# Optimization experiments

Measured on AMD Instinct MI355X. Metric: run time of the kernel, lower is better.

The kernel has to match this reference:

```python
import jax, jax.numpy as jnp
import numpy as np

N, IN_C, HID, OUT_C = 100000, 512, 256, 32
E = 1_600_000
K, LAM1, LAM2 = 5, 3.0, 3.0  # elastic prop hyperparams


def setup_inputs() -> dict:
    key = jax.random.key(0)
    ks = jax.random.split(key, 6)
    x = jax.random.normal(ks[0], (N, IN_C), dtype=jnp.float32)
    edge_index = jax.random.randint(ks[1], (2, E), 0, N, dtype=jnp.int64)
    s1 = 1.0 / np.sqrt(IN_C)
    s2 = 1.0 / np.sqrt(HID)
    W1 = jax.random.uniform(ks[2], (IN_C, HID), jnp.float32, -s1, s1)
    b1 = jax.random.uniform(ks[3], (HID,), jnp.float32, -s1, s1)
    W2 = jax.random.uniform(ks[4], (HID, OUT_C), jnp.float32, -s2, s2)
    b2 = jax.random.uniform(ks[5], (OUT_C,), jnp.float32, -s2, s2)
    return dict(x=x, edge_index=edge_index, W1=W1, b1=b1, W2=W2, b2=b2)


def _emp(h, row, col):
    """Elastic Message Passing (ElasticGNN): proximal-gradient iterations over
    the degree-normalized incidence operator with L1 dual projection."""
    n = h.shape[0]
    deg = jnp.zeros((n,), h.dtype).at[row].add(1.0).at[col].add(1.0)
    dis = jax.lax.rsqrt(jnp.maximum(deg, 1.0))  # 1/sqrt(deg)
    dr = dis[row][:, None]  # [E,1]
    dc = dis[col][:, None]
    gamma = 1.0 / (1.0 + LAM2)
    beta = 1.0 / (2.0 * gamma)

    def step(carry, _):
        z, y = carry
        # dual ascent on edge variables: z += beta * (Delta y), then project
        # onto the L-inf ball of radius lambda1 (prox of L1 penalty's dual)
        z = jnp.clip(z + beta * (y[row] * dr - y[col] * dc), -LAM1, LAM1)
        # primal: y = gamma * h - gamma * Delta^T z  (scatter back to nodes)
        atz = jnp.zeros_like(y).at[row].add(z * dr).at[col].add(-(z * dc))
        y = gamma * h - gamma * atz
        return (z, y), None

    z0 = jnp.zeros((row.shape[0], h.shape[1]), h.dtype)
    (z, y), _ = jax.lax.scan(step, (z0, gamma * h), None, length=K)
    return y


def reference(x, edge_index, W1, b1, W2, b2):
    # eval mode: dropout is identity
    h = jax.nn.relu(x @ W1 + b1)
    h = h @ W2 + b2                       # [N, OUT_C]
    row, col = edge_index[0], edge_index[1]
    y = _emp(h, row, col)                 # sparse elastic propagation
    return jax.nn.log_softmax(y, axis=1)
```

## Files before the change

### kernel.cpp

```cpp
#include <hip/hip_runtime.h>
#include <math.h>

#define IN_C  512
#define HID   256
#define OUT_C 32
#define GAMMA 0.25f
#define BETA  2.0f
#define LAM1  3.0f
#define ZS    10922.0f
#define ZSI   (1.0f / 10922.0f)

#define BM 128
#define BN 128
#define BK 16

__global__ __launch_bounds__(256) void gemm1_relu_kernel(
    const float* __restrict__ A, const float* __restrict__ B,
    const float* __restrict__ bias, float* __restrict__ C, int M)
{
    __shared__ float As[BK][BM + 4];
    __shared__ float Bs[BK][BN + 4];
    const int tid = threadIdx.x;
    const int bm = blockIdx.x * BM;
    const int bn = blockIdx.y * BN;
    const int tx = tid & 15;
    const int ty = tid >> 4;

    float acc[8][8];
#pragma unroll
    for (int i = 0; i < 8; ++i)
#pragma unroll
        for (int j = 0; j < 8; ++j) acc[i][j] = 0.f;

    const int a_row = tid >> 2;
    const int a_col = (tid & 3) << 2;
    const int b_row = tid >> 5;
    const int b_col = (tid & 31) << 2;

    for (int k0 = 0; k0 < IN_C; k0 += BK) {
#pragma unroll
        for (int r = 0; r < 2; ++r) {
            const int m = a_row + r * 64;
            const int gm = bm + m;
            float4 v = make_float4(0.f, 0.f, 0.f, 0.f);
            if (gm < M) v = *(const float4*)&A[(size_t)gm * IN_C + k0 + a_col];
            As[a_col + 0][m] = v.x;
            As[a_col + 1][m] = v.y;
            As[a_col + 2][m] = v.z;
            As[a_col + 3][m] = v.w;
        }
#pragma unroll
        for (int r = 0; r < 2; ++r) {
            const int kk = b_row + r * 8;
            *(float4*)&Bs[kk][b_col] =
                *(const float4*)&B[(size_t)(k0 + kk) * HID + bn + b_col];
        }
        __syncthreads();
#pragma unroll
        for (int kk = 0; kk < BK; ++kk) {
            float a[8], b[8];
            *(float4*)&a[0] = *(float4*)&As[kk][ty * 8];
            *(float4*)&a[4] = *(float4*)&As[kk][ty * 8 + 4];
            *(float4*)&b[0] = *(float4*)&Bs[kk][tx * 4];
            *(float4*)&b[4] = *(float4*)&Bs[kk][64 + tx * 4];
#pragma unroll
            for (int i = 0; i < 8; ++i)
#pragma unroll
                for (int j = 0; j < 8; ++j)
                    acc[i][j] = fmaf(a[i], b[j], acc[i][j]);
        }
        __syncthreads();
    }

#pragma unroll
    for (int i = 0; i < 8; ++i) {
        const int gm = bm + ty * 8 + i;
        if (gm >= M) continue;
#pragma unroll
        for (int g = 0; g < 2; ++g) {
            const int gn = bn + g * 64 + tx * 4;
            float4 v;
            v.x = fmaxf(acc[i][g * 4 + 0] + bias[gn + 0], 0.f);
            v.y = fmaxf(acc[i][g * 4 + 1] + bias[gn + 1], 0.f);
            v.z = fmaxf(acc[i][g * 4 + 2] + bias[gn + 2], 0.f);
            v.w = fmaxf(acc[i][g * 4 + 3] + bias[gn + 3], 0.f);
            *(float4*)&C[(size_t)gm * HID + gn] = v;
        }
    }
}

#define G2_ROWS 128
#define G2_KT   64

__global__ __launch_bounds__(256) void gemm2_kernel(
    const float* __restrict__ H1, const float* __restrict__ W2,
    const float* __restrict__ b2, float* __restrict__ H,
    float* __restrict__ Y, int M)
{
    __shared__ float W2s[HID * OUT_C];
    __shared__ float rows_s[G2_ROWS][G2_KT + 4];
    const int tid = threadIdx.x;
    const int brow = blockIdx.x * G2_ROWS;
    const int cg = tid & 7;
    const int rg = tid >> 3;

#pragma unroll
    for (int r = 0; r < 8; ++r)
        ((float4*)W2s)[tid + r * 256] = ((const float4*)W2)[tid + r * 256];

    float acc[4][4];
#pragma unroll
    for (int r = 0; r < 4; ++r)
#pragma unroll
        for (int c = 0; c < 4; ++c) acc[r][c] = 0.f;

    for (int k0 = 0; k0 < HID; k0 += G2_KT) {
        __syncthreads();
#pragma unroll
        for (int i = 0; i < 8; ++i) {
            const int idx = tid + i * 256;
            const int rl = idx >> 4;
            const int c4 = idx & 15;
            const int gr = brow + rl;
            float4 v = make_float4(0.f, 0.f, 0.f, 0.f);
            if (gr < M) v = *(const float4*)&H1[(size_t)gr * HID + k0 + c4 * 4];
            *(float4*)&rows_s[rl][c4 * 4] = v;
        }
        __syncthreads();
#pragma unroll
        for (int kq = 0; kq < G2_KT / 4; ++kq) {
            float4 w[4];
#pragma unroll
            for (int j = 0; j < 4; ++j)
                w[j] = ((const float4*)W2s)[(k0 + kq * 4 + j) * 8 + cg];
#pragma unroll
            for (int r = 0; r < 4; ++r) {
                const float4 rh = *(const float4*)&rows_s[rg * 4 + r][kq * 4];
                acc[r][0] = fmaf(rh.x, w[0].x, acc[r][0]);
                acc[r][1] = fmaf(rh.x, w[0].y, acc[r][1]);
                acc[r][2] = fmaf(rh.x, w[0].z, acc[r][2]);
                acc[r][3] = fmaf(rh.x, w[0].w, acc[r][3]);
                acc[r][0] = fmaf(rh.y, w[1].x, acc[r][0]);
                acc[r][1] = fmaf(rh.y, w[1].y, acc[r][1]);
                acc[r][2] = fmaf(rh.y, w[1].z, acc[r][2]);
                acc[r][3] = fmaf(rh.y, w[1].w, acc[r][3]);
                acc[r][0] = fmaf(rh.z, w[2].x, acc[r][0]);
                acc[r][1] = fmaf(rh.z, w[2].y, acc[r][1]);
                acc[r][2] = fmaf(rh.z, w[2].z, acc[r][2]);
                acc[r][3] = fmaf(rh.z, w[2].w, acc[r][3]);
                acc[r][0] = fmaf(rh.w, w[3].x, acc[r][0]);
                acc[r][1] = fmaf(rh.w, w[3].y, acc[r][1]);
                acc[r][2] = fmaf(rh.w, w[3].z, acc[r][2]);
                acc[r][3] = fmaf(rh.w, w[3].w, acc[r][3]);
            }
        }
    }

    const float4 bias = *(const float4*)&b2[cg * 4];
#pragma unroll
    for (int r = 0; r < 4; ++r) {
        const int grow = brow + rg * 4 + r;
        if (grow >= M) continue;
        float4 s;
        s.x = acc[r][0] + bias.x;
        s.y = acc[r][1] + bias.y;
        s.z = acc[r][2] + bias.z;
        s.w = acc[r][3] + bias.w;
        *(float4*)&H[(size_t)grow * OUT_C + cg * 4] = s;
        float4 y0;
        y0.x = GAMMA * s.x; y0.y = GAMMA * s.y;
        y0.z = GAMMA * s.z; y0.w = GAMMA * s.w;
        *(float4*)&Y[(size_t)grow * OUT_C + cg * 4] = y0;
    }
}

__global__ void hist2_kernel(const int* __restrict__ row, const int* __restrict__ col,
                             int* __restrict__ cnt_r, int* __restrict__ cnt_c, int E)
{
    const int t = blockIdx.x * blockDim.x + threadIdx.x;
    if (t >= E) return;
    atomicAdd(&cnt_r[row[t]], 1);
    atomicAdd(&cnt_c[col[t]], 1);
}

__global__ void dis_kernel(const int* __restrict__ cnt_r, const int* __restrict__ cnt_c,
                           float* __restrict__ dis, int N)
{
    const int t = blockIdx.x * blockDim.x + threadIdx.x;
    if (t < N) dis[t] = 1.f / sqrtf(fmaxf((float)(cnt_r[t] + cnt_c[t]), 1.f));
}

#define SCAN_CHUNK 1024

__global__ __launch_bounds__(256) void scan1_kernel(
    const int* __restrict__ counts, int* __restrict__ bsum, int N)
{
    __shared__ int sm[256];
    const int tid = threadIdx.x;
    const int base = blockIdx.x * SCAN_CHUNK + tid * 4;
    int s = 0;
#pragma unroll
    for (int i = 0; i < 4; ++i)
        if (base + i < N) s += counts[base + i];
    sm[tid] = s;
    __syncthreads();
    for (int off = 128; off; off >>= 1) {
        if (tid < off) sm[tid] += sm[tid + off];
        __syncthreads();
    }
    if (tid == 0) bsum[blockIdx.x] = sm[0];
}

__global__ void scan2_kernel(int* __restrict__ bsum, int* __restrict__ boff, int nb)
{
    if (threadIdx.x == 0 && blockIdx.x == 0) {
        int acc = 0;
        for (int i = 0; i < nb; ++i) { boff[i] = acc; acc += bsum[i]; }
    }
}

__global__ __launch_bounds__(256) void scan3_kernel(
    const int* __restrict__ counts, const int* __restrict__ boff,
    int* __restrict__ ptr, int* __restrict__ cursor, int N)
{
    __shared__ int sm[256];
    const int tid = threadIdx.x;
    const int base = blockIdx.x * SCAN_CHUNK + tid * 4;
    int c[4];
#pragma unroll
    for (int i = 0; i < 4; ++i)
        c[i] = (base + i < N) ? counts[base + i] : 0;
    const int tsum = c[0] + c[1] + c[2] + c[3];
    sm[tid] = tsum;
    __syncthreads();
    for (int off = 1; off < 256; off <<= 1) {
        int v = (tid >= off) ? sm[tid - off] : 0;
        __syncthreads();
        sm[tid] += v;
        __syncthreads();
    }
    int run = boff[blockIdx.x] + sm[tid] - tsum;
#pragma unroll
    for (int i = 0; i < 4; ++i) {
        if (base + i < N) {
            ptr[base + i] = run;
            cursor[base + i] = run;
        }
        run += c[i];
    }
}

__global__ void scatter2_kernel(const int* __restrict__ row, const int* __restrict__ col,
                                int* __restrict__ cur_r, int* __restrict__ cur_c,
                                int* __restrict__ col_s, int2* __restrict__ entries_c, int E)
{
    const int t = blockIdx.x * blockDim.x + threadIdx.x;
    if (t >= E) return;
    const int r = row[t], c = col[t];
    const int nid = atomicAdd(&cur_r[r], 1);
    col_s[nid] = c;
    const int pc = atomicAdd(&cur_c[c], 1);
    entries_c[pc] = make_int2(nid, r);
}

__device__ __forceinline__ float clip1(float v)
{
    return fminf(fmaxf(v, -LAM1), LAM1);
}

__device__ __forceinline__ float4 zload4(const short* p)
{
    const short4 s = *(const short4*)p;
    return make_float4(s.x * ZSI, s.y * ZSI, s.z * ZSI, s.w * ZSI);
}

__device__ __forceinline__ void zstore4(short* p, float4 z)
{
    short4 s;
    s.x = (short)__float2int_rn(z.x * ZS);
    s.y = (short)__float2int_rn(z.y * ZS);
    s.z = (short)__float2int_rn(z.z * ZS);
    s.w = (short)__float2int_rn(z.w * ZS);
    *(short4*)p = s;
}

template <bool FIRST, bool LAST>
__global__ __launch_bounds__(256) void emp_kernel(
    const int* __restrict__ rowptr, const int* __restrict__ cnt_r,
    const int* __restrict__ col_s,
    const int* __restrict__ colptr, const int* __restrict__ cnt_c,
    const int2* __restrict__ entries_c,
    const short* __restrict__ zin, short* __restrict__ zout,
    const float* __restrict__ dis, const float* __restrict__ H,
    const float* __restrict__ Yold, float* __restrict__ Ynew,
    float* __restrict__ OUT, int N)
{
    const int t = blockIdx.x * 256 + threadIdx.x;
    const int n = t >> 3;
    if (n >= N) return;
    const int c4 = (t & 7) << 2;
    const float dn = dis[n];
    const float4 ys = *(const float4*)&Yold[(size_t)n * OUT_C + c4];
    const float4 ysdn = make_float4(ys.x * dn, ys.y * dn, ys.z * dn, ys.w * dn);

    float4 acc = make_float4(0.f, 0.f, 0.f, 0.f);

    {
        const int b = rowptr[n];
        const int d = cnt_r[n];
        for (int i = 0; i < d; ++i) {
            const int e = b + i;
            const int other = col_s[e];
            const float dt = dis[other];
            const float4 yo = *(const float4*)&Yold[(size_t)other * OUT_C + c4];
            float4 z;
            if (FIRST) z = make_float4(0.f, 0.f, 0.f, 0.f);
            else       z = zload4(&zin[(size_t)e * OUT_C + c4]);
            z.x = clip1(z.x + BETA * (ysdn.x - yo.x * dt));
            z.y = clip1(z.y + BETA * (ysdn.y - yo.y * dt));
            z.z = clip1(z.z + BETA * (ysdn.z - yo.z * dt));
            z.w = clip1(z.w + BETA * (ysdn.w - yo.w * dt));
            acc.x += z.x; acc.y += z.y; acc.z += z.z; acc.w += z.w;
            if (!LAST) zstore4(&zout[(size_t)e * OUT_C + c4], z);
        }
    }

    {
        const int b = colptr[n];
        const int d = cnt_c[n];
        for (int i = 0; i < d; ++i) {
            const int2 en = entries_c[b + i];
            const float dt = dis[en.y];
            const float4 yo = *(const float4*)&Yold[(size_t)en.y * OUT_C + c4];
            float4 z;
            if (FIRST) z = make_float4(0.f, 0.f, 0.f, 0.f);
            else       z = zload4(&zin[(size_t)en.x * OUT_C + c4]);
            z.x = clip1(z.x + BETA * (yo.x * dt - ysdn.x));
            z.y = clip1(z.y + BETA * (yo.y * dt - ysdn.y));
            z.z = clip1(z.z + BETA * (yo.z * dt - ysdn.z));
            z.w = clip1(z.w + BETA * (yo.w * dt - ysdn.w));
            acc.x -= z.x; acc.y -= z.y; acc.z -= z.z; acc.w -= z.w;
        }
    }

    const float4 h4 = *(const float4*)&H[(size_t)n * OUT_C + c4];
    float4 v;
    v.x = GAMMA * (h4.x - dn * acc.x);
    v.y = GAMMA * (h4.y - dn * acc.y);
    v.z = GAMMA * (h4.z - dn * acc.z);
    v.w = GAMMA * (h4.w - dn * acc.w);

    if (!LAST) {
        *(float4*)&Ynew[(size_t)n * OUT_C + c4] = v;
    } else {
        float m = fmaxf(fmaxf(v.x, v.y), fmaxf(v.z, v.w));
#pragma unroll
        for (int off = 4; off; off >>= 1) m = fmaxf(m, __shfl_xor(m, off, 8));
        float sum = expf(v.x - m) + expf(v.y - m) + expf(v.z - m) + expf(v.w - m);
#pragma unroll
        for (int off = 4; off; off >>= 1) sum += __shfl_xor(sum, off, 8);
        const float lse = m + logf(sum);
        float4 o;
        o.x = v.x - lse; o.y = v.y - lse; o.z = v.z - lse; o.w = v.w - lse;
        *(float4*)&OUT[(size_t)n * OUT_C + c4] = o;
    }
}

extern "C" void kernel_launch(void* const* d_in, const int* in_sizes, int n_in,
                              void* d_out, int out_size, void* d_ws, size_t ws_size,
                              hipStream_t stream)
{
    const float* x  = (const float*)d_in[0];
    const int*   ei = (const int*)d_in[1];
    const float* W1 = (const float*)d_in[2];
    const float* b1 = (const float*)d_in[3];
    const float* W2 = (const float*)d_in[4];
    const float* b2 = (const float*)d_in[5];
    const int M = in_sizes[0] / IN_C;
    const int E = in_sizes[1] / 2;
    const int* row = ei;
    const int* col = ei + E;

    char* ws = (char*)d_ws;
    short* zA = (short*)ws;
    short* zB = zA + (size_t)E * OUT_C;
    float* h1 = (float*)ws;
    float* h  = (float*)(zB + (size_t)E * OUT_C);
    float* y0 = h  + (size_t)M * OUT_C;
    float* y1 = y0 + (size_t)M * OUT_C;
    int* cnt_r   = (int*)(y1 + (size_t)M * OUT_C);
    int* cnt_c   = cnt_r + M;
    int* rowptr  = cnt_c + M;
    int* colptr  = rowptr + M;
    int* cur_r   = colptr + M;
    int* cur_c   = cur_r + M;
    float* dis   = (float*)(cur_c + M);
    const int nb = (M + SCAN_CHUNK - 1) / SCAN_CHUNK;
    int* bsum    = (int*)(dis + M);
    int* boff    = bsum + nb;
    int* col_s   = boff + nb;
    int2* entries_c = (int2*)(col_s + E);

    hipMemsetAsync(cnt_r, 0, 2 * (size_t)M * sizeof(int), stream);

    dim3 g1((M + BM - 1) / BM, HID / BN);
    gemm1_relu_kernel<<<g1, 256, 0, stream>>>(x, W1, b1, h1, M);
    gemm2_kernel<<<(M + G2_ROWS - 1) / G2_ROWS, 256, 0, stream>>>(h1, W2, b2, h, y0, M);

    hist2_kernel<<<(E + 255) / 256, 256, 0, stream>>>(row, col, cnt_r, cnt_c, E);
    dis_kernel<<<(M + 255) / 256, 256, 0, stream>>>(cnt_r, cnt_c, dis, M);
    scan1_kernel<<<nb, 256, 0, stream>>>(cnt_r, bsum, M);
    scan2_kernel<<<1, 64, 0, stream>>>(bsum, boff, nb);
    scan3_kernel<<<nb, 256, 0, stream>>>(cnt_r, boff, rowptr, cur_r, M);
    scan1_kernel<<<nb, 256, 0, stream>>>(cnt_c, bsum, M);
    scan2_kernel<<<1, 64, 0, stream>>>(bsum, boff, nb);
    scan3_kernel<<<nb, 256, 0, stream>>>(cnt_c, boff, colptr, cur_c, M);
    scatter2_kernel<<<(E + 255) / 256, 256, 0, stream>>>(row, col, cur_r, cur_c,
                                                         col_s, entries_c, E);

    const int nblocks = (M * 8 + 255) / 256;
    emp_kernel<true, false><<<nblocks, 256, 0, stream>>>(
        rowptr, cnt_r, col_s, colptr, cnt_c, entries_c,
        (const short*)nullptr, zA, dis, h, y0, y1, nullptr, M);
    emp_kernel<false, false><<<nblocks, 256, 0, stream>>>(
        rowptr, cnt_r, col_s, colptr, cnt_c, entries_c,
        zA, zB, dis, h, y1, y0, nullptr, M);
    emp_kernel<false, false><<<nblocks, 256, 0, stream>>>(
        rowptr, cnt_r, col_s, colptr, cnt_c, entries_c,
        zB, zA, dis, h, y0, y1, nullptr, M);
    emp_kernel<false, false><<<nblocks, 256, 0, stream>>>(
        rowptr, cnt_r, col_s, colptr, cnt_c, entries_c,
        zA, zB, dis, h, y1, y0, nullptr, M);
    emp_kernel<false, true><<<nblocks, 256, 0, stream>>>(
        rowptr, cnt_r, col_s, colptr, cnt_c, entries_c,
        zB, nullptr, dis, h, y0, nullptr, (float*)d_out, M);
}
```

Before: 1.705 ms.

## Store edge duals twice in row- and col-sorted order for contiguous access

```diff
diff --git a/kernel.cpp b/kernel.cpp
--- a/kernel.cpp
+++ b/kernel.cpp
@@ -252,7 +252,7 @@
 
 __global__ void scatter2_kernel(const int* __restrict__ row, const int* __restrict__ col,
                                 int* __restrict__ cur_r, int* __restrict__ cur_c,
-                                int* __restrict__ col_s, int2* __restrict__ entries_c, int E)
+                                int* __restrict__ col_s, int* __restrict__ row_s, int E)
 {
     const int t = blockIdx.x * blockDim.x + threadIdx.x;
     if (t >= E) return;
@@ -260,7 +260,7 @@
     const int nid = atomicAdd(&cur_r[r], 1);
     col_s[nid] = c;
     const int pc = atomicAdd(&cur_c[c], 1);
-    entries_c[pc] = make_int2(nid, r);
+    row_s[pc] = r;
 }
 
 __device__ __forceinline__ float clip1(float v)
@@ -289,8 +289,8 @@
     const int* __restrict__ rowptr, const int* __restrict__ cnt_r,
     const int* __restrict__ col_s,
     const int* __restrict__ colptr, const int* __restrict__ cnt_c,
-    const int2* __restrict__ entries_c,
-    const short* __restrict__ zin, short* __restrict__ zout,
+    const int* __restrict__ row_s,
+    short* __restrict__ zr, short* __restrict__ zc,
     const float* __restrict__ dis, const float* __restrict__ H,
     const float* __restrict__ Yold, float* __restrict__ Ynew,
     float* __restrict__ OUT, int N)
@@ -315,13 +315,13 @@
             const float4 yo = *(const float4*)&Yold[(size_t)other * OUT_C + c4];
             float4 z;
             if (FIRST) z = make_float4(0.f, 0.f, 0.f, 0.f);
-            else       z = zload4(&zin[(size_t)e * OUT_C + c4]);
+            else       z = zload4(&zr[(size_t)e * OUT_C + c4]);
             z.x = clip1(z.x + BETA * (ysdn.x - yo.x * dt));
             z.y = clip1(z.y + BETA * (ysdn.y - yo.y * dt));
             z.z = clip1(z.z + BETA * (ysdn.z - yo.z * dt));
             z.w = clip1(z.w + BETA * (ysdn.w - yo.w * dt));
             acc.x += z.x; acc.y += z.y; acc.z += z.z; acc.w += z.w;
-            if (!LAST) zstore4(&zout[(size_t)e * OUT_C + c4], z);
+            if (!LAST) zstore4(&zr[(size_t)e * OUT_C + c4], z);
         }
     }
 
@@ -329,17 +329,19 @@
         const int b = colptr[n];
         const int d = cnt_c[n];
         for (int i = 0; i < d; ++i) {
-            const int2 en = entries_c[b + i];
-            const float dt = dis[en.y];
-            const float4 yo = *(const float4*)&Yold[(size_t)en.y * OUT_C + c4];
+            const int p = b + i;
+            const int other = row_s[p];
+            const float dt = dis[other];
+            const float4 yo = *(const float4*)&Yold[(size_t)other * OUT_C + c4];
             float4 z;
             if (FIRST) z = make_float4(0.f, 0.f, 0.f, 0.f);
-            else       z = zload4(&zin[(size_t)en.x * OUT_C + c4]);
+            else       z = zload4(&zc[(size_t)p * OUT_C + c4]);
             z.x = clip1(z.x + BETA * (yo.x * dt - ysdn.x));
             z.y = clip1(z.y + BETA * (yo.y * dt - ysdn.y));
             z.z = clip1(z.z + BETA * (yo.z * dt - ysdn.z));
             z.w = clip1(z.w + BETA * (yo.w * dt - ysdn.w));
             acc.x -= z.x; acc.y -= z.y; acc.z -= z.z; acc.w -= z.w;
+            if (!LAST) zstore4(&zc[(size_t)p * OUT_C + c4], z);
         }
     }
 
@@ -382,10 +384,10 @@
     const int* col = ei + E;
 
     char* ws = (char*)d_ws;
-    short* zA = (short*)ws;
-    short* zB = zA + (size_t)E * OUT_C;
+    short* zr = (short*)ws;
+    short* zc = zr + (size_t)E * OUT_C;
     float* h1 = (float*)ws;
-    float* h  = (float*)(zB + (size_t)E * OUT_C);
+    float* h  = (float*)(zc + (size_t)E * OUT_C);
     float* y0 = h  + (size_t)M * OUT_C;
     float* y1 = y0 + (size_t)M * OUT_C;
     int* cnt_r   = (int*)(y1 + (size_t)M * OUT_C);
@@ -399,7 +401,7 @@
     int* bsum    = (int*)(dis + M);
     int* boff    = bsum + nb;
     int* col_s   = boff + nb;
-    int2* entries_c = (int2*)(col_s + E);
+    int* row_s   = col_s + E;
 
     hipMemsetAsync(cnt_r, 0, 2 * (size_t)M * sizeof(int), stream);
 
@@ -416,22 +418,22 @@
     scan2_kernel<<<1, 64, 0, stream>>>(bsum, boff, nb);
     scan3_kernel<<<nb, 256, 0, stream>>>(cnt_c, boff, colptr, cur_c, M);
     scatter2_kernel<<<(E + 255) / 256, 256, 0, stream>>>(row, col, cur_r, cur_c,
-                                                         col_s, entries_c, E);
+                                                         col_s, row_s, E);
 
     const int nblocks = (M * 8 + 255) / 256;
     emp_kernel<true, false><<<nblocks, 256, 0, stream>>>(
-        rowptr, cnt_r, col_s, colptr, cnt_c, entries_c,
-        (const short*)nullptr, zA, dis, h, y0, y1, nullptr, M);
+        rowptr, cnt_r, col_s, colptr, cnt_c, row_s,
+        zr, zc, dis, h, y0, y1, nullptr, M);
     emp_kernel<false, false><<<nblocks, 256, 0, stream>>>(
-        rowptr, cnt_r, col_s, colptr, cnt_c, entries_c,
-        zA, zB, dis, h, y1, y0, nullptr, M);
+        rowptr, cnt_r, col_s, colptr, cnt_c, row_s,
+        zr, zc, dis, h, y1, y0, nullptr, M);
     emp_kernel<false, false><<<nblocks, 256, 0, stream>>>(
-        rowptr, cnt_r, col_s, colptr, cnt_c, entries_c,
-        zB, zA, dis, h, y0, y1, nullptr, M);
+        rowptr, cnt_r, col_s, colptr, cnt_c, row_s,
+        zr, zc, dis, h, y0, y1, nullptr, M);
     emp_kernel<false, false><<<nblocks, 256, 0, stream>>>(
-        rowptr, cnt_r, col_s, colptr, cnt_c, entries_c,
-        zA, zB, dis, h, y1, y0, nullptr, M);
+        rowptr, cnt_r, col_s, colptr, cnt_c, row_s,
+        zr, zc, dis, h, y1, y0, nullptr, M);
     emp_kernel<false, true><<<nblocks, 256, 0, stream>>>(
-        rowptr, cnt_r, col_s, colptr, cnt_c, entries_c,
-        zB, nullptr, dis, h, y0, nullptr, (float*)d_out, M);
-}
+        rowptr, cnt_r, col_s, colptr, cnt_c, row_s,
+        zr, zc, dis, h, y0, nullptr, (float*)d_out, M);
+}
```

Measured after the change: 1.720 ms. About the same (+0.8%).
